# Kernel optimization log

Hardware: AMD Instinct MI355X
Metric: run time of the kernel (lower is better)

## Reference

```python
import jax, jax.numpy as jnp
import numpy as np


def conv_t(x, w, stride, padding):
    """torch.nn.functional.conv_transpose2d equivalent.
    w is in torch ConvTranspose2d layout [C_in, C_out, kh, kw]."""
    k = w.shape[2]
    kern = jnp.flip(w, (2, 3)).transpose(1, 0, 2, 3)  # -> OIHW
    pad = k - 1 - padding
    return jax.lax.conv_general_dilated(
        x, kern,
        window_strides=(1, 1),
        padding=[(pad, pad), (pad, pad)],
        lhs_dilation=(stride, stride),
        dimension_numbers=('NCHW', 'OIHW', 'NCHW'))


def setup_inputs() -> dict:
    key = jax.random.key(0)
    ks = jax.random.split(key, 4)
    B, planes, inplanes, H = 32, 256, 128, 28
    x = jax.random.normal(ks[0], (B, planes, H, H), dtype=jnp.float32)
    # torch ConvTranspose2d weight layout: [in, out, kh, kw]
    w_conv2 = jax.random.normal(ks[1], (planes, planes, 3, 3), dtype=jnp.float32) * 0.02
    w_conv1 = jax.random.normal(ks[2], (planes, inplanes, 3, 3), dtype=jnp.float32) * 0.02
    w_up = jax.random.normal(ks[3], (planes // 2, inplanes, 2, 2), dtype=jnp.float32) * 0.02
    # Fixup init: biases zero, scale one
    z = jnp.zeros((1,), dtype=jnp.float32)
    return {
        'x': x, 'w_conv2': w_conv2, 'w_conv1': w_conv1, 'w_up': w_up,
        'bias1a': z, 'bias1b': z, 'bias2a': z, 'bias2b': z,
        'scale': jnp.ones((1,), dtype=jnp.float32),
    }


def reference(x, w_conv2, w_conv1, w_up, bias1a, bias1b, bias2a, bias2b, scale):
    # main branch
    out = conv_t(x + bias1a, w_conv2, stride=1, padding=1)        # [B,planes,H,W]
    out = jax.nn.relu(out + bias1b)
    out = conv_t(out + bias2a, w_conv1, stride=2, padding=1)      # [B,inplanes,2H-1,2W-1]
    out = out * scale + bias2b

    # upsample branch: keep the C/2 channels with the largest (max - min) range,
    # per sample, in ascending-range order (matches np.argsort(diff)[C/2:]).
    C = x.shape[1]
    rng = jnp.max(x, axis=(2, 3)) - jnp.min(x, axis=(2, 3))       # [B,C]
    idx = jnp.argsort(rng, axis=1)[:, C // 2:]                    # [B,C/2]
    x_sel = jnp.take_along_axis(x, idx[:, :, None, None], axis=1)  # [B,C/2,H,W]
    identity = conv_t(x_sel + bias1a, w_up, stride=2, padding=0)  # [B,inplanes,2H,2W]

    # pad main branch top-left by 1 to match 2H x 2W
    out = jnp.pad(out, ((0, 0), (0, 0), (1, 0), (1, 0)))
    out = jax.nn.relu(out + identity)
    return out
```

## Files before the change

### kernel.cpp

```cpp
#include <hip/hip_runtime.h>

#define NB 32
#define NC 256
#define NO 128
#define HH 28
#define HW 784
#define OH 56

typedef unsigned short u16;
typedef unsigned int u32;
typedef __attribute__((ext_vector_type(8))) short bf16x8;
typedef __attribute__((ext_vector_type(4))) float f32x4;
typedef __attribute__((ext_vector_type(8))) unsigned short u16x8;

#define MFMA(A,B,C) __builtin_amdgcn_mfma_f32_16x16x32_bf16(A,B,C,0,0,0)

typedef __attribute__((address_space(3))) u32 lds_u32;
typedef const __attribute__((address_space(1))) u32 glb_u32;

__device__ __forceinline__ void gld_lds16(const void* g, void* l) {
    __builtin_amdgcn_global_load_lds((glb_u32*)g, (lds_u32*)l, 16, 0, 0);
}

__device__ __forceinline__ u16 f2bf(float f) {
    unsigned u = __float_as_uint(f);
    unsigned r = (u + 0x7fffu + ((u >> 16) & 1u)) >> 16;
    return (u16)r;
}

__global__ __launch_bounds__(256) void k_prep(
    const float* __restrict__ x, const float* __restrict__ pb1a,
    u16* __restrict__ xT2, float* __restrict__ rng,
    const float* __restrict__ w2, const float* __restrict__ w1,
    const float* __restrict__ wup,
    u16* __restrict__ wT2, u16* __restrict__ wc2T,
    u16* __restrict__ wupT, uint4* __restrict__ r1T4)
{
    __shared__ float sx[8][HW];
    __shared__ float smx[8][4], smn[8][4];

    if (blockIdx.x >= 1024) {
        int blk = blockIdx.x - 1024;
        if (blk < 288) {
            int g = blk * 256 + threadIdx.x;
            int o = g & 255;
            int cb = (g >> 8) & 31;
            int tap = g >> 13;
            int u = 2 - tap / 3, v = 2 - tap % 3;
            u16x8 out;
#pragma unroll
            for (int ci = 0; ci < 8; ++ci) {
                int c = cb * 8 + ci;
                out[ci] = f2bf(w2[((c * NC + o) * 3 + u) * 3 + v]);
            }
            *(u16x8*)(wT2 + (size_t)g * 8) = out;
        } else if (blk < 432) {
            const int taps[9] = {0, 2, 6, 8, 1, 7, 3, 5, 4};
            int g = (blk - 288) * 256 + threadIdx.x;
            int o = g & 127;
            int cb = (g >> 7) & 31;
            int s = g >> 12;
            int tap = taps[s];
            u16x8 out;
#pragma unroll
            for (int ci = 0; ci < 8; ++ci) {
                int c = cb * 8 + ci;
                out[ci] = f2bf(w1[(c * NO + o) * 9 + tap]);
            }
            *(u16x8*)(wc2T + (size_t)g * 8) = out;
        } else if (blk < 464) {
            int g = (blk - 432) * 256 + threadIdx.x;
            int o = g & 127;
            int kb = (g >> 7) & 15;
            int p = g >> 11;
            u16x8 out;
#pragma unroll
            for (int ki = 0; ki < 8; ++ki) {
                int k = kb * 8 + ki;
                out[ki] = f2bf(wup[(k * NO + o) * 4 + p]);
            }
            *(u16x8*)(wupT + (size_t)g * 8) = out;
        } else {
            int g = (blk - 464) * 256 + threadIdx.x;
            int i = g % 176;
            int bc = g / 176;
            int b = bc >> 5, cb = bc & 31;
            int row, cx;
            if (i < 32)      { row = 0;  cx = i; }
            else if (i < 64) { row = 29; cx = i - 32; }
            else {
                int j = i - 64;
                row = 1 + (j >> 2);
                int k = j & 3;
                cx = (k == 0) ? 0 : 28 + k;
            }
            r1T4[((b * 30 + row) * 32 + cb) * 32 + cx] = make_uint4(0, 0, 0, 0);
        }
        return;
    }

    int t = threadIdx.x;
    int b = blockIdx.x >> 5, cb = blockIdx.x & 31;
    float b1a = pb1a[0];
    const float* xb = x + ((size_t)b * NC + cb * 8) * HW;

    float mx[8], mn[8];
#pragma unroll
    for (int ci = 0; ci < 8; ++ci) { mx[ci] = -1e30f; mn[ci] = 1e30f; }
#pragma unroll
    for (int ci = 0; ci < 8; ++ci) {
        const float4* xb4 = (const float4*)(xb + ci * HW);
        float4* sx4 = (float4*)sx[ci];
        if (t < 196) {
            float4 v = xb4[t];
            sx4[t] = v;
            mx[ci] = fmaxf(fmaxf(v.x, v.y), fmaxf(v.z, v.w));
            mn[ci] = fminf(fminf(v.x, v.y), fminf(v.z, v.w));
        }
    }
    int lane = t & 63, wv = t >> 6;
#pragma unroll
    for (int ci = 0; ci < 8; ++ci) {
        float a = mx[ci], i = mn[ci];
        for (int off = 32; off; off >>= 1) {
            a = fmaxf(a, __shfl_down(a, off, 64));
            i = fminf(i, __shfl_down(i, off, 64));
        }
        if (lane == 0) { smx[ci][wv] = a; smn[ci][wv] = i; }
    }
    __syncthreads();
    if (t < 8) {
        float a = fmaxf(fmaxf(smx[t][0], smx[t][1]), fmaxf(smx[t][2], smx[t][3]));
        float i = fminf(fminf(smn[t][0], smn[t][1]), fminf(smn[t][2], smn[t][3]));
        rng[b * NC + cb * 8 + t] = a - i;
    }
    for (int g = t; g < 960; g += 256) {
        int ry = g >> 5, cx = g & 31;
        int y = ry - 1, xx = cx - 1;
        bool valid = (y >= 0 && y < HH && xx >= 0 && xx < HH);
        u16x8 out;
#pragma unroll
        for (int ci = 0; ci < 8; ++ci) {
            float f = valid ? sx[ci][y * 28 + xx] + b1a : 0.f;
            out[ci] = f2bf(f);
        }
        *(u16x8*)(xT2 + ((((size_t)b * 30 + ry) * 32 + cb) * 32 + cx) * 8) = out;
    }
}

__global__ __launch_bounds__(512, 4) void k_conv1x(
    const u16* __restrict__ xT2, const u16* __restrict__ wT2,
    const float* __restrict__ pb1b, const float* __restrict__ pb2a,
    u16* __restrict__ r1T,
    const float* __restrict__ x, const float* __restrict__ rng,
    const float* __restrict__ pb1a, u16* __restrict__ xupT)
{
    __shared__ u16 sA[6 * 16 * 32 * 8];
    if (blockIdx.x >= 448) {
        int blk = blockIdx.x - 448;
        int tid = threadIdx.x;
        int b = blk / 28;
        int qy = blk - b * 28;
        float b1a = pb1a[0];

        float* srng = (float*)sA;
        int* ssel = (int*)(sA + 2048);

        if (tid < 256) srng[tid] = rng[b * NC + tid];
        __syncthreads();
        if (tid < 256) {
            float v = srng[tid];
            int rank = 0;
            for (int j = 0; j < NC; ++j) {
                float u = srng[j];
                rank += (u < v) || (u == v && j < tid);
            }
            if (rank >= NC / 2) ssel[rank - NC / 2] = tid;
        }
        __syncthreads();

        int cx = tid & 31;
        int kb = tid >> 5;
        bool valid = cx < 28;
        const float* xb = x + (size_t)b * NC * HW + qy * 28 + (valid ? cx : 0);
        u16x8 out;
#pragma unroll
        for (int ki = 0; ki < 8; ++ki) {
            int ch = ssel[kb * 8 + ki];
            float f = valid ? xb[ch * HW] + b1a : 0.f;
            out[ki] = f2bf(f);
        }
        size_t g = ((size_t)(b * 28 + qy) * 16 + kb) * 32 + cx;
        *(u16x8*)(xupT + g * 8) = out;
        return;
    }

    int tid = threadIdx.x;
    int wave = tid >> 6, lane = tid & 63;
    int wpi = wave >> 2;
    int wo = wave & 3;
    int l15 = lane & 15, lg = lane >> 4;

    int idx = blockIdx.x;
    int b = idx / 14;
    int rem = idx - b * 14;
    int rg = rem >> 1;
    int og = rem & 1;
    int y0 = rg * 4;

    float b1b = pb1b[0], b2a = pb2a[0];

    int bOff[2];
#pragma unroll
    for (int ot = 0; ot < 2; ++ot)
        bOff[ot] = (lg * 256 + (og * 128 + wo * 32 + ot * 16 + l15)) * 16;

    f32x4 acc[4][2] = {};
    const char* wq = (const char*)wT2;
    const char* ap0 = (const char*)sA;
    const uint4* gx = (const uint4*)xT2;
    uint4* dst = (uint4*)sA;

    int aLane = (2 * wpi) * 8192 + lg * 512 + l15 * 16;

    for (int half = 0; half < 2; ++half) {
        if (half) __syncthreads();
#pragma unroll
        for (int i = 0; i < 6; ++i)
            gld_lds16(gx + (b * 30 + y0 + i) * 1024 + half * 512 + tid,
                      dst + tid + i * 512);
        __syncthreads();

        for (int cc = 0; cc < 128; cc += 32) {
            int c0 = half * 128 + cc;
            int aBase = aLane + cc * 64;
#pragma unroll
            for (int dx = 0; dx < 3; ++dx) {
                bf16x8 w[3][2];
#pragma unroll
                for (int dy = 0; dy < 3; ++dy)
#pragma unroll
                    for (int ot = 0; ot < 2; ++ot)
                        w[dy][ot] = *(const bf16x8*)(wq +
                            (bOff[ot] + (dy * 3 + dx) * 131072 + c0 * 512));
                bf16x8 a[4][2];
#pragma unroll
                for (int r = 0; r < 4; ++r)
#pragma unroll
                    for (int h = 0; h < 2; ++h)
                        a[r][h] = *(const bf16x8*)(ap0 +
                            (aBase + r * 8192 + (h * 16 + dx) * 16));
#pragma unroll
                for (int dy = 0; dy < 3; ++dy)
#pragma unroll
                    for (int m = 0; m < 2; ++m)
#pragma unroll
                        for (int h = 0; h < 2; ++h)
#pragma unroll
                            for (int ot = 0; ot < 2; ++ot)
                                acc[m * 2 + h][ot] =
                                    MFMA(a[m + dy][h], w[dy][ot], acc[m * 2 + h][ot]);
            }
        }
    }

#pragma unroll
    for (int m = 0; m < 2; ++m)
#pragma unroll
        for (int h = 0; h < 2; ++h) {
            int y = y0 + 2 * wpi + m;
            int x0 = h * 16 + lg * 4;
            if (x0 >= 28) continue;
#pragma unroll
            for (int ot = 0; ot < 2; ++ot) {
                int o = og * 128 + wo * 32 + ot * 16 + l15;
                size_t base = ((((size_t)b * 30 + y + 1) * 32 + (o >> 3)) * 32 + (x0 + 1)) * 8 + (o & 7);
#pragma unroll
                for (int r = 0; r < 4; ++r) {
                    float f = fmaxf(acc[m * 2 + h][ot][r] + b1b, 0.f) + b2a;
                    r1T[base + (size_t)r * 8] = f2bf(f);
                }
            }
        }
}

__global__ __launch_bounds__(512, 2) void k_conv2_mfma(
    const u16* __restrict__ r1T, const u16* __restrict__ xupT,
    const u16* __restrict__ wc2T, const u16* __restrict__ wupT,
    const float* __restrict__ pscale, const float* __restrict__ pb2b,
    float* __restrict__ out)
{
    __shared__ uint4 sA2[5120];
    int tid = threadIdx.x;
    int wave = tid >> 6, lane = tid & 63;
    int wpi = wave >> 2;
    int wo = wave & 3;
    int l15 = lane & 15, lg = lane >> 4;

    int b = blockIdx.x / 7;
    int rg = blockIdx.x - b * 7;
    int y0 = rg * 4;

    float scale = pscale[0], b2b = pb2b[0];

    {
        const uint4* src = (const uint4*)(r1T + (size_t)(b * 30 + y0) * 8192);
#pragma unroll
        for (int i = 0; i < 10; ++i)
            gld_lds16(src + tid + i * 512, sA2 + tid + i * 512);
    }
    __syncthreads();

    f32x4 acc[4][4][2] = {};

    const char* sp = (const char*)sA2;
    const char* wp = (const char*)wc2T;

    int aBase[4];
#pragma unroll
    for (int pt = 0; pt < 4; ++pt) {
        int rel = 2 * wpi + (pt >> 1) + 1;
        int qt = pt & 1;
        aBase[pt] = ((rel * 32 + lg) * 32 + (qt * 16 + l15 + 1)) * 16;
    }
    int bBase = (lg * 128 + wo * 32 + l15) * 16;

    for (int c0 = 0; c0 < 256; c0 += 32) {
        bf16x8 w[9][2];
#pragma unroll
        for (int s = 0; s < 9; ++s)
#pragma unroll
            for (int ot = 0; ot < 2; ++ot)
                w[s][ot] = *(const bf16x8*)(wp + (bBase + s * 65536 + c0 * 256 + ot * 256));
#pragma unroll
        for (int pt = 0; pt < 4; ++pt) {
            const char* ap = sp + (aBase[pt] + c0 * 64);
            bf16x8 aD = *(const bf16x8*)(ap);
            bf16x8 aC = *(const bf16x8*)(ap - 16);
            bf16x8 aB = *(const bf16x8*)(ap - 16384);
            bf16x8 aA = *(const bf16x8*)(ap - 16400);
#pragma unroll
            for (int ot = 0; ot < 2; ++ot) {
                acc[0][pt][ot] = MFMA(aD, w[0][ot], acc[0][pt][ot]);
                acc[0][pt][ot] = MFMA(aC, w[1][ot], acc[0][pt][ot]);
                acc[0][pt][ot] = MFMA(aB, w[2][ot], acc[0][pt][ot]);
                acc[0][pt][ot] = MFMA(aA, w[3][ot], acc[0][pt][ot]);
                acc[1][pt][ot] = MFMA(aD, w[4][ot], acc[1][pt][ot]);
                acc[1][pt][ot] = MFMA(aB, w[5][ot], acc[1][pt][ot]);
                acc[2][pt][ot] = MFMA(aD, w[6][ot], acc[2][pt][ot]);
                acc[2][pt][ot] = MFMA(aC, w[7][ot], acc[2][pt][ot]);
                acc[3][pt][ot] = MFMA(aD, w[8][ot], acc[3][pt][ot]);
            }
        }
    }

#pragma unroll
    for (int pt = 0; pt < 4; ++pt) {
        int qy = y0 + 2 * wpi + (pt >> 1);
        int qt = pt & 1;
        int qx0 = qt * 16 + lg * 4;
        bool zr = (qy == 0);
#pragma unroll
        for (int ot = 0; ot < 2; ++ot)
#pragma unroll
            for (int r = 0; r < 4; ++r) {
                bool zc = (qx0 + r == 0);
                float a0 = acc[0][pt][ot][r], a1 = acc[1][pt][ot][r];
                float a2 = acc[2][pt][ot][r], a3 = acc[3][pt][ot][r];
                acc[0][pt][ot][r] = (zr || zc) ? 0.f : fmaf(a0, scale, b2b);
                acc[1][pt][ot][r] = zr ? 0.f : fmaf(a1, scale, b2b);
                acc[2][pt][ot][r] = zc ? 0.f : fmaf(a2, scale, b2b);
                acc[3][pt][ot][r] = fmaf(a3, scale, b2b);
            }
    }

    const char* up = (const char*)xupT;
    const char* wu = (const char*)wupT;
    int uBaseA[4];
#pragma unroll
    for (int pt = 0; pt < 4; ++pt) {
        int qy = y0 + 2 * wpi + (pt >> 1);
        int qt = pt & 1;
        uBaseA[pt] = (((b * 28 + qy) * 16 + lg) * 32 + (qt * 16 + l15)) * 16;
    }
    for (int k0 = 0; k0 < 128; k0 += 32) {
        bf16x8 wb[4][2];
#pragma unroll
        for (int p = 0; p < 4; ++p)
#pragma unroll
            for (int ot = 0; ot < 2; ++ot)
                wb[p][ot] = *(const bf16x8*)(wu + (bBase + p * 32768 + k0 * 256 + ot * 256));
#pragma unroll
        for (int pt = 0; pt < 4; ++pt) {
            bf16x8 aU = *(const bf16x8*)(up + (uBaseA[pt] + k0 * 64));
#pragma unroll
            for (int p = 0; p < 4; ++p)
#pragma unroll
                for (int ot = 0; ot < 2; ++ot)
                    acc[p][pt][ot] = MFMA(aU, wb[p][ot], acc[p][pt][ot]);
        }
    }

#pragma unroll
    for (int pt = 0; pt < 4; ++pt) {
        int qy = y0 + 2 * wpi + (pt >> 1);
        int qt = pt & 1;
        int qx0 = qt * 16 + lg * 4;
        if (qx0 >= 28) continue;
#pragma unroll
        for (int ot = 0; ot < 2; ++ot) {
            int o = wo * 32 + ot * 16 + l15;
            size_t base = ((size_t)(b * NO + o) * OH + 2 * qy) * OH + 2 * qx0;
#pragma unroll
            for (int r = 0; r < 4; ++r) {
                float2 v0 = { fmaxf(acc[0][pt][ot][r], 0.f), fmaxf(acc[1][pt][ot][r], 0.f) };
                float2 v1 = { fmaxf(acc[2][pt][ot][r], 0.f), fmaxf(acc[3][pt][ot][r], 0.f) };
                *reinterpret_cast<float2*>(&out[base + 2 * r]) = v0;
                *reinterpret_cast<float2*>(&out[base + OH + 2 * r]) = v1;
            }
        }
    }
}

extern "C" void kernel_launch(void* const* d_in, const int* in_sizes, int n_in,
                              void* d_out, int out_size, void* d_ws, size_t ws_size,
                              hipStream_t stream)
{
    const float* x     = (const float*)d_in[0];
    const float* w2    = (const float*)d_in[1];
    const float* w1    = (const float*)d_in[2];
    const float* wup   = (const float*)d_in[3];
    const float* b1a   = (const float*)d_in[4];
    const float* b1b   = (const float*)d_in[5];
    const float* b2a   = (const float*)d_in[6];
    const float* b2b   = (const float*)d_in[7];
    const float* scale = (const float*)d_in[8];

    char* ws = (char*)d_ws;
    u16* xT2   = (u16*)(ws);
    u16* r1T   = (u16*)(ws + 15728640);
    u16* xupT  = (u16*)(ws + 31457280);
    u16* wT2   = (u16*)(ws + 38797312);
    u16* wc2T  = (u16*)(ws + 39976960);
    u16* wupT  = (u16*)(ws + 40566784);
    float* rng = (float*)(ws + 40697856);
    float* out = (float*)d_out;

    hipLaunchKernelGGL(k_prep, dim3(2192), dim3(256), 0, stream,
                       x, b1a, xT2, rng, w2, w1, wup, wT2, wc2T, wupT, (uint4*)r1T);
    hipLaunchKernelGGL(k_conv1x, dim3(1344), dim3(512), 0, stream,
                       xT2, wT2, b1b, b2a, r1T, x, rng, b1a, xupT);
    hipLaunchKernelGGL(k_conv2_mfma, dim3(NB * 7), dim3(512), 0, stream,
                       r1T, xupT, wc2T, wupT, scale, b2b, out);
}
```

Measured before the change: 92.47 us.

## Switch conv1 kernel to 32x32x16 MFMA tiles with 256-thread blocks

Rewrites the first transposed-conv kernel to use 32x32x16 bf16 MFMA instead of 16x16x32. Each wave now covers 32 pixels by 64 output channels, and the block shrinks to 4 waves. The larger tiles are meant to cut LDS and weight loads per MFMA and raise arithmetic intensity. The cost is more accumulator registers, a strided epilogue with a bounds mask, and fewer threads per block to stage the same LDS tile.

```diff
diff --git a/kernel.cpp b/kernel.cpp
--- a/kernel.cpp
+++ b/kernel.cpp
@@ -11,9 +11,11 @@
 typedef unsigned int u32;
 typedef __attribute__((ext_vector_type(8))) short bf16x8;
 typedef __attribute__((ext_vector_type(4))) float f32x4;
+typedef __attribute__((ext_vector_type(16))) float f32x16;
 typedef __attribute__((ext_vector_type(8))) unsigned short u16x8;
 
-#define MFMA(A,B,C) __builtin_amdgcn_mfma_f32_16x16x32_bf16(A,B,C,0,0,0)
+#define MFMA(A,B,C)   __builtin_amdgcn_mfma_f32_16x16x32_bf16(A,B,C,0,0,0)
+#define MFMA32(A,B,C) __builtin_amdgcn_mfma_f32_32x32x16_bf16(A,B,C,0,0,0)
 
 typedef __attribute__((address_space(3))) u32 lds_u32;
 typedef const __attribute__((address_space(1))) u32 glb_u32;
@@ -148,7 +150,7 @@
     }
 }
 
-__global__ __launch_bounds__(512, 4) void k_conv1x(
+__global__ __launch_bounds__(256, 3) void k_conv1x(
     const u16* __restrict__ xT2, const u16* __restrict__ wT2,
     const float* __restrict__ pb1b, const float* __restrict__ pb2a,
     u16* __restrict__ r1T,
@@ -166,9 +168,9 @@
         float* srng = (float*)sA;
         int* ssel = (int*)(sA + 2048);
 
-        if (tid < 256) srng[tid] = rng[b * NC + tid];
+        srng[tid] = rng[b * NC + tid];
         __syncthreads();
-        if (tid < 256) {
+        {
             float v = srng[tid];
             int rank = 0;
             for (int j = 0; j < NC; ++j) {
@@ -179,27 +181,31 @@
         }
         __syncthreads();
 
-        int cx = tid & 31;
-        int kb = tid >> 5;
-        bool valid = cx < 28;
-        const float* xb = x + (size_t)b * NC * HW + qy * 28 + (valid ? cx : 0);
-        u16x8 out;
-#pragma unroll
-        for (int ki = 0; ki < 8; ++ki) {
-            int ch = ssel[kb * 8 + ki];
-            float f = valid ? xb[ch * HW] + b1a : 0.f;
-            out[ki] = f2bf(f);
-        }
-        size_t g = ((size_t)(b * 28 + qy) * 16 + kb) * 32 + cx;
-        *(u16x8*)(xupT + g * 8) = out;
+#pragma unroll
+        for (int it = 0; it < 2; ++it) {
+            int g = it * 256 + tid;
+            int cx = g & 31;
+            int kb = g >> 5;
+            bool valid = cx < 28;
+            const float* xb = x + (size_t)b * NC * HW + qy * 28 + (valid ? cx : 0);
+            u16x8 out;
+#pragma unroll
+            for (int ki = 0; ki < 8; ++ki) {
+                int ch = ssel[kb * 8 + ki];
+                float f = valid ? xb[ch * HW] + b1a : 0.f;
+                out[ki] = f2bf(f);
+            }
+            size_t gg = ((size_t)(b * 28 + qy) * 16 + kb) * 32 + cx;
+            *(u16x8*)(xupT + gg * 8) = out;
+        }
         return;
     }
 
     int tid = threadIdx.x;
     int wave = tid >> 6, lane = tid & 63;
-    int wpi = wave >> 2;
-    int wo = wave & 3;
-    int l15 = lane & 15, lg = lane >> 4;
+    int q = wave >> 1;
+    int wn = wave & 1;
+    int l31 = lane & 31, hi = lane >> 5;
 
     int idx = blockIdx.x;
     int b = idx / 14;
@@ -210,78 +216,72 @@
 
     float b1b = pb1b[0], b2a = pb2a[0];
 
-    int bOff[2];
-#pragma unroll
-    for (int ot = 0; ot < 2; ++ot)
-        bOff[ot] = (lg * 256 + (og * 128 + wo * 32 + ot * 16 + l15)) * 16;
-
-    f32x4 acc[4][2] = {};
+    int bBase[2];
+#pragma unroll
+    for (int j = 0; j < 2; ++j)
+        bBase[j] = hi * 4096 + (og * 128 + wn * 64 + j * 32 + l31) * 16;
+
+    f32x16 acc[2][2] = {};
     const char* wq = (const char*)wT2;
     const char* ap0 = (const char*)sA;
     const uint4* gx = (const uint4*)xT2;
     uint4* dst = (uint4*)sA;
 
-    int aLane = (2 * wpi) * 8192 + lg * 512 + l15 * 16;
+    int aLane = q * 2 * 8192 + hi * 512 + l31 * 16;
 
     for (int half = 0; half < 2; ++half) {
         if (half) __syncthreads();
 #pragma unroll
-        for (int i = 0; i < 6; ++i)
-            gld_lds16(gx + (b * 30 + y0 + i) * 1024 + half * 512 + tid,
-                      dst + tid + i * 512);
+        for (int i = 0; i < 12; ++i)
+            gld_lds16(gx + (b * 30 + y0 + (i >> 1)) * 1024 + half * 512 + (i & 1) * 256 + tid,
+                      dst + i * 256 + tid);
         __syncthreads();
 
-        for (int cc = 0; cc < 128; cc += 32) {
+        for (int cc = 0; cc < 128; cc += 16) {
             int c0 = half * 128 + cc;
-            int aBase = aLane + cc * 64;
+            int aB = aLane + cc * 64;
+            int wB = (c0 >> 3) * 4096;
 #pragma unroll
             for (int dx = 0; dx < 3; ++dx) {
                 bf16x8 w[3][2];
 #pragma unroll
                 for (int dy = 0; dy < 3; ++dy)
 #pragma unroll
-                    for (int ot = 0; ot < 2; ++ot)
-                        w[dy][ot] = *(const bf16x8*)(wq +
-                            (bOff[ot] + (dy * 3 + dx) * 131072 + c0 * 512));
-                bf16x8 a[4][2];
+                    for (int j = 0; j < 2; ++j)
+                        w[dy][j] = *(const bf16x8*)(wq +
+                            ((dy * 3 + dx) * 131072 + wB + bBase[j]));
+                bf16x8 a[4];
 #pragma unroll
                 for (int r = 0; r < 4; ++r)
-#pragma unroll
-                    for (int h = 0; h < 2; ++h)
-                        a[r][h] = *(const bf16x8*)(ap0 +
-                            (aBase + r * 8192 + (h * 16 + dx) * 16));
+                    a[r] = *(const bf16x8*)(ap0 + (aB + r * 8192 + dx * 16));
 #pragma unroll
                 for (int dy = 0; dy < 3; ++dy)
 #pragma unroll
                     for (int m = 0; m < 2; ++m)
 #pragma unroll
-                        for (int h = 0; h < 2; ++h)
-#pragma unroll
-                            for (int ot = 0; ot < 2; ++ot)
-                                acc[m * 2 + h][ot] =
-                                    MFMA(a[m + dy][h], w[dy][ot], acc[m * 2 + h][ot]);
-            }
-        }
-    }
-
-#pragma unroll
-    for (int m = 0; m < 2; ++m)
-#pragma unroll
-        for (int h = 0; h < 2; ++h) {
-            int y = y0 + 2 * wpi + m;
-            int x0 = h * 16 + lg * 4;
-            if (x0 >= 28) continue;
-#pragma unroll
-            for (int ot = 0; ot < 2; ++ot) {
-                int o = og * 128 + wo * 32 + ot * 16 + l15;
-                size_t base = ((((size_t)b * 30 + y + 1) * 32 + (o >> 3)) * 32 + (x0 + 1)) * 8 + (o & 7);
-#pragma unroll
-                for (int r = 0; r < 4; ++r) {
-                    float f = fmaxf(acc[m * 2 + h][ot][r] + b1b, 0.f) + b2a;
-                    r1T[base + (size_t)r * 8] = f2bf(f);
+                        for (int j = 0; j < 2; ++j)
+                            acc[m][j] = MFMA32(a[m + dy], w[dy][j], acc[m][j]);
+            }
+        }
+    }
+
+#pragma unroll
+    for (int m = 0; m < 2; ++m) {
+        int y = y0 + 2 * q + m;
+#pragma unroll
+        for (int j = 0; j < 2; ++j) {
+            int o = og * 128 + wn * 64 + j * 32 + l31;
+            size_t obase = (((size_t)b * 30 + y + 1) * 32 + (o >> 3)) * 32;
+#pragma unroll
+            for (int r = 0; r < 16; ++r) {
+                int i = (r & 3) + 8 * (r >> 2) + 4 * hi;
+                if (i < 28) {
+                    float f = fmaxf(acc[m][j][r] + b1b, 0.f) + b2a;
+                    r1T[(obase + i + 1) * 8 + (o & 7)] = f2bf(f);
                 }
             }
         }
+    }
 }
 
 __global__ __launch_bounds__(512, 2) void k_conv2_mfma(
@@ -448,7 +448,7 @@
 
     hipLaunchKernelGGL(k_prep, dim3(2192), dim3(256), 0, stream,
                        x, b1a, xT2, rng, w2, w1, wup, wT2, wc2T, wupT, (uint4*)r1T);
-    hipLaunchKernelGGL(k_conv1x, dim3(1344), dim3(512), 0, stream,
+    hipLaunchKernelGGL(k_conv1x, dim3(1344), dim3(256), 0, stream,
                        xT2, wT2, b1b, b2a, r1T, x, rng, b1a, xupT);
     hipLaunchKernelGGL(k_conv2_mfma, dim3(NB * 7), dim3(512), 0, stream,
                        r1T, xupT, wc2T, wupT, scale, b2b, out);
```

Result: slower. 102.6 us (+11.0%).
